# Performance work log

Hardware: AMD Instinct MI355X
Metric: run time of the kernel (lower is better)

The kernel has to match this reference:

```python
import jax, jax.numpy as jnp
import numpy as np


def setup_inputs() -> dict:
    key = jax.random.key(0)
    kq, kk, kv = jax.random.split(key, 3)
    B, S, H, D = 2, 2048, 32, 128
    q = jax.random.normal(kq, (B, S, H, D), dtype=jnp.float32)
    k = jax.random.normal(kk, (B, S, H, D), dtype=jnp.float32)
    v = jax.random.normal(kv, (B, S, H, D), dtype=jnp.float32)
    return {"q": q, "k": k, "v": v}


def _causal_attention(q, k, v):
    # q,k,v: [B, S, H, D] (flash-attn layout). Zigzag ring attention computes
    # exactly standard causal attention; zigzag only balances work across ranks.
    B, S, H, D = q.shape
    scale = 1.0 / jnp.sqrt(jnp.asarray(D, q.dtype))
    scores = jnp.einsum('bqhd,bkhd->bhqk', q, k) * scale  # [B,H,S,S]
    causal = jnp.tril(jnp.ones((S, S), dtype=bool))
    scores = jnp.where(causal, scores, jnp.finfo(scores.dtype).min)
    probs = jax.nn.softmax(scores, axis=-1)
    return jnp.einsum('bhqk,bkhd->bqhd', probs, v)  # [B,S,H,D]


def reference(q, k, v):
    out = _causal_attention(q, k, v)
    return jnp.sum(out)
```

## Files before the change

kernel.cpp:

```cpp
#include <hip/hip_runtime.h>
#include <hip/hip_bf16.h>
#include <stdint.h>

#define B_ 2
#define S_ 2048
#define H_ 32
#define D_ 128
#define R_ (B_*H_*S_)
#define QKB (B_ * S_ * (H_/8))
#define VSB (B_ * S_)
#define NDB (2 * R_ / 1024)
#define CPB 40

typedef __bf16 bf16x8 __attribute__((ext_vector_type(8)));
typedef float  f32x16 __attribute__((ext_vector_type(16)));

#if __has_builtin(__builtin_amdgcn_exp2f)
#define EXP2F(x) __builtin_amdgcn_exp2f(x)
#else
#define EXP2F(x) exp2f(x)
#endif

#define AS1 __attribute__((address_space(1)))
#define AS3 __attribute__((address_space(3)))

__device__ __forceinline__ unsigned short f2bf(float f) {
  unsigned u = __float_as_uint(f);
  u += 0x7FFFu + ((u >> 16) & 1u);
  return (unsigned short)(u >> 16);
}

__global__ __launch_bounds__(256) void prep(
    const float* __restrict__ q, const float* __restrict__ k,
    const float* __restrict__ v,
    unsigned short* __restrict__ qb, unsigned short* __restrict__ kb,
    float* __restrict__ vsum, float* __restrict__ nd, float* __restrict__ out0) {
  const int bid = blockIdx.x;
  const int t = threadIdx.x;
  if (bid == 0 && t == 0) out0[0] = 0.f;
  if (bid < 2 * QKB) {
    const int which = bid >= QKB;
    const int i2 = which ? bid - QKB : bid;
    const float* src = which ? k : q;
    unsigned short* dst = which ? kb : qb;
    const float sc = which ? 1.0f : 0.0883883476483184f * 1.4426950408889634f;
    const int b   = i2 / (S_ * 4);
    const int rem = i2 % (S_ * 4);
    const int s   = rem >> 2;
    const int h   = (rem & 3) * 8 + (t >> 5);
    const int lane32 = t & 31;
    const float4 v4 = *reinterpret_cast<const float4*>(
        src + (((size_t)b * S_ + s) * H_ + h) * D_ + lane32 * 4);
    ushort4 o;
    o.x = f2bf(v4.x * sc); o.y = f2bf(v4.y * sc);
    o.z = f2bf(v4.z * sc); o.w = f2bf(v4.w * sc);
    *reinterpret_cast<ushort4*>(
        dst + (((size_t)b * H_ + h) * S_ + s) * D_ + lane32 * 4) = o;
  } else if (bid < 2 * QKB + VSB) {
    const int i2 = bid - 2 * QKB;
    const int b = i2 / S_, s = i2 % S_;
    const int h = t >> 3, i = t & 7;
    const float* p = v + (((size_t)b * S_ + s) * H_ + h) * D_ + i * 16;
    const float4 a0 = *reinterpret_cast<const float4*>(p + 0);
    const float4 a1 = *reinterpret_cast<const float4*>(p + 4);
    const float4 a2 = *reinterpret_cast<const float4*>(p + 8);
    const float4 a3 = *reinterpret_cast<const float4*>(p + 12);
    float sum = (a0.x+a0.y+a0.z+a0.w) + (a1.x+a1.y+a1.z+a1.w)
              + (a2.x+a2.y+a2.z+a2.w) + (a3.x+a3.y+a3.z+a3.w);
    sum += __shfl_xor(sum, 1);
    sum += __shfl_xor(sum, 2);
    sum += __shfl_xor(sum, 4);
    if (i == 0) vsum[((size_t)b * H_ + h) * S_ + s] = sum;
  } else {
    float4* p = reinterpret_cast<float4*>(nd);
    p[(size_t)(bid - 2 * QKB - VSB) * 256 + t] = float4{0.f, 0.f, 0.f, 0.f};
  }
}

__global__ __launch_bounds__(256, 4) void attn_sum(
    const unsigned short* __restrict__ qg_, const unsigned short* __restrict__ kg_,
    const float* __restrict__ vsum, float* __restrict__ numb,
    float* __restrict__ denb) {
  __shared__ uint4 kbuf[2][1024];
  __shared__ float vsbuf[2][64];

  const int id = blockIdx.x;
  const int y  = id >> 3;
  const int bh = (id & 7) + 8 * (y / CPB);
  const int c  = y % CPB;

  int qt, h, nch;
  if (c < 4)       { qt = c;                 h = 0;            nch = 1; }
  else if (c < 12) { qt = 4 + ((c - 4) >> 1);  h = (c - 4) & 1;  nch = 2; }
  else if (c < 24) { qt = 8 + (c - 12) / 3;    h = (c - 12) % 3; nch = 3; }
  else             { qt = 12 + ((c - 24) >> 2); h = (c - 24) & 3; nch = 4; }
  const int nkt  = 2 * qt + 2;
  const int bas_ = nkt / nch, rem = nkt % nch;
  const int kt0  = h * bas_ + (h < rem ? h : rem);
  const int kt1  = kt0 + bas_ + (h < rem ? 1 : 0);

  const int t  = threadIdx.x;
  const int w  = t >> 6;
  const int l  = t & 63;
  const int ln = l & 31, l5 = l >> 5;

  const size_t base = (size_t)bh * S_ * D_;
  const int qrow0 = qt * 128 + w * 32;
  const unsigned short* ksrc0 = kg_ + base;
  const float* vsrc0 = vsum + (size_t)bh * S_;

  bf16x8 qfrag[8];
  {
    const unsigned short* qp = qg_ + base + (size_t)(qrow0 + ln) * D_ + l5 * 8;
    #pragma unroll
    for (int kb8 = 0; kb8 < 8; ++kb8)
      qfrag[kb8] = *reinterpret_cast<const bf16x8*>(qp + kb8 * 16);
  }

  auto stage = [&](int j, int slot) {
    const unsigned short* ksrc = ksrc0 + (size_t)j * 64 * D_;
    #pragma unroll
    for (int i = 0; i < 4; ++i) {
      const int idx = w * 256 + i * 64 + l;
      const int r   = idx >> 4;
      const int p   = idx & 15;
      const int cc  = p ^ (r & 15);
      const unsigned short* src = ksrc + r * D_ + cc * 8;
      __builtin_amdgcn_global_load_lds(
          (const AS1 void*)src, (AS3 void*)(&kbuf[slot][idx & ~63]), 16, 0, 0);
    }
    __builtin_amdgcn_global_load_lds(
        (const AS1 void*)(vsrc0 + j * 64 + l), (AS3 void*)(&vsbuf[slot][0]), 4, 0, 0);
  };

  float num[16], den[16];
  #pragma unroll
  for (int r = 0; r < 16; ++r) { num[r] = 0.f; den[r] = 0.f; }

  stage(kt0, 0);
  int cur = 0;
  const int xr = ln & 15;
  for (int kt = kt0; kt < kt1; ++kt) {
    asm volatile("s_waitcnt vmcnt(0)" ::: "memory");
    __syncthreads();
    if (kt + 1 < kt1) stage(kt + 1, cur ^ 1);

    const int ktb = kt * 64;
    if (ktb <= qrow0 + 31) {
      #pragma unroll
      for (int nb = 0; nb < 2; ++nb) {
        const int kbase = ktb + nb * 32;
        if (kbase > qrow0 + 31) continue;
        const uint4* rowb = &kbuf[cur][(nb * 32 + ln) * 16];
        f32x16 sacc = {0.f,0.f,0.f,0.f,0.f,0.f,0.f,0.f,
                       0.f,0.f,0.f,0.f,0.f,0.f,0.f,0.f};
        __builtin_amdgcn_s_setprio(1);
        #pragma unroll
        for (int kb8 = 0; kb8 < 8; ++kb8) {
          const bf16x8 bf = *reinterpret_cast<const bf16x8*>(&rowb[(kb8 * 2 + l5) ^ xr]);
          sacc = __builtin_amdgcn_mfma_f32_32x32x16_bf16(qfrag[kb8], bf, sacc, 0, 0, 0);
        }
        __builtin_amdgcn_s_setprio(0);
        const float vsv = vsbuf[cur][nb * 32 + ln];
        if (kbase + 31 <= qrow0) {
          #pragma unroll
          for (int r = 0; r < 16; ++r) {
            const float e = EXP2F(sacc[r]);
            den[r] += e;
            num[r] = fmaf(e, vsv, num[r]);
          }
        } else {
          const int kgc = kbase + ln;
          #pragma unroll
          for (int r = 0; r < 16; ++r) {
            const int qgr = qrow0 + (r & 3) + 8 * (r >> 2) + 4 * l5;
            const float e = (kgc <= qgr) ? EXP2F(sacc[r]) : 0.f;
            den[r] += e;
            num[r] = fmaf(e, vsv, num[r]);
          }
        }
      }
    }
    cur ^= 1;
  }

  #pragma unroll
  for (int m = 1; m < 32; m <<= 1) {
    #pragma unroll
    for (int r = 0; r < 16; ++r) {
      num[r] += __shfl_xor(num[r], m);
      den[r] += __shfl_xor(den[r], m);
    }
  }
  if (ln == 0) {
    float* nrow = numb + (size_t)bh * S_;
    float* drow = denb + (size_t)bh * S_;
    #pragma unroll
    for (int r = 0; r < 16; ++r) {
      const int qgr = qrow0 + (r & 3) + 8 * (r >> 2) + 4 * l5;
      atomicAdd(&nrow[qgr], num[r]);
      atomicAdd(&drow[qgr], den[r]);
    }
  }
}

__global__ __launch_bounds__(256) void finalize(
    const float* __restrict__ numb, const float* __restrict__ denb,
    float* __restrict__ out) {
  const int i = blockIdx.x * 256 + threadIdx.x;
  float c = numb[i] / denb[i];
  #pragma unroll
  for (int m = 1; m < 64; m <<= 1) c += __shfl_xor(c, m);
  __shared__ float ps[4];
  if ((threadIdx.x & 63) == 0) ps[threadIdx.x >> 6] = c;
  __syncthreads();
  if (threadIdx.x == 0) atomicAdd(out, ps[0] + ps[1] + ps[2] + ps[3]);
}

extern "C" void kernel_launch(void* const* d_in, const int* in_sizes, int n_in,
                              void* d_out, int out_size, void* d_ws, size_t ws_size,
                              hipStream_t stream) {
  const float* q = (const float*)d_in[0];
  const float* k = (const float*)d_in[1];
  const float* v = (const float*)d_in[2];
  float* out = (float*)d_out;

  unsigned short* qb = (unsigned short*)d_ws;
  unsigned short* kb = qb + (size_t)R_ * D_;
  float* vsum = (float*)(kb + (size_t)R_ * D_);
  float* numb = vsum + R_;
  float* denb = numb + R_;

  hipLaunchKernelGGL(prep, dim3(2 * QKB + VSB + NDB), dim3(256), 0, stream,
                     q, k, v, qb, kb, vsum, numb, out);
  hipLaunchKernelGGL(attn_sum, dim3(64 * CPB), dim3(256), 0, stream,
                     qb, kb, vsum, numb, denb);
  hipLaunchKernelGGL(finalize, dim3(R_ / 256), dim3(256), 0, stream,
                     numb, denb, out);
}
```

Baseline: 114.4 us.

## Use 4-slot 32-row K pipeline with partial waits and grid-stride prep kernel

```diff
diff --git a/kernel.cpp b/kernel.cpp
--- a/kernel.cpp
+++ b/kernel.cpp
@@ -7,9 +7,9 @@
 #define H_ 32
 #define D_ 128
 #define R_ (B_*H_*S_)
-#define QKB (B_ * S_ * (H_/8))
-#define VSB (B_ * S_)
-#define NDB (2 * R_ / 1024)
+#define PG 2048
+#define QKU (2 * B_ * S_ * (H_/8))
+#define VSU (B_ * S_)
 #define CPB 40
 
 typedef __bf16 bf16x8 __attribute__((ext_vector_type(8)));
@@ -38,9 +38,12 @@
   const int bid = blockIdx.x;
   const int t = threadIdx.x;
   if (bid == 0 && t == 0) out0[0] = 0.f;
-  if (bid < 2 * QKB) {
-    const int which = bid >= QKB;
-    const int i2 = which ? bid - QKB : bid;
+
+  #pragma unroll 4
+  for (int g = 0; g < QKU / PG; ++g) {
+    const int u = bid + g * PG;
+    const int which = u >= (QKU / 2);
+    const int i2 = which ? u - (QKU / 2) : u;
     const float* src = which ? k : q;
     unsigned short* dst = which ? kb : qb;
     const float sc = which ? 1.0f : 0.0883883476483184f * 1.4426950408889634f;
@@ -56,9 +59,12 @@
     o.z = f2bf(v4.z * sc); o.w = f2bf(v4.w * sc);
     *reinterpret_cast<ushort4*>(
         dst + (((size_t)b * H_ + h) * S_ + s) * D_ + lane32 * 4) = o;
-  } else if (bid < 2 * QKB + VSB) {
-    const int i2 = bid - 2 * QKB;
-    const int b = i2 / S_, s = i2 % S_;
+  }
+
+  #pragma unroll
+  for (int g = 0; g < VSU / PG; ++g) {
+    const int u = bid + g * PG;
+    const int b = u / S_, s = u % S_;
     const int h = t >> 3, i = t & 7;
     const float* p = v + (((size_t)b * S_ + s) * H_ + h) * D_ + i * 16;
     const float4 a0 = *reinterpret_cast<const float4*>(p + 0);
@@ -71,9 +77,11 @@
     sum += __shfl_xor(sum, 2);
     sum += __shfl_xor(sum, 4);
     if (i == 0) vsum[((size_t)b * H_ + h) * S_ + s] = sum;
-  } else {
+  }
+
+  if (bid < 256) {
     float4* p = reinterpret_cast<float4*>(nd);
-    p[(size_t)(bid - 2 * QKB - VSB) * 256 + t] = float4{0.f, 0.f, 0.f, 0.f};
+    p[(size_t)bid * 256 + t] = float4{0.f, 0.f, 0.f, 0.f};
   }
 }
 
@@ -81,8 +89,8 @@
     const unsigned short* __restrict__ qg_, const unsigned short* __restrict__ kg_,
     const float* __restrict__ vsum, float* __restrict__ numb,
     float* __restrict__ denb) {
-  __shared__ uint4 kbuf[2][1024];
-  __shared__ float vsbuf[2][64];
+  __shared__ uint4 kbuf[4][512];
+  __shared__ float vsbuf[4][64];
 
   const int id = blockIdx.x;
   const int y  = id >> 3;
@@ -98,6 +106,7 @@
   const int bas_ = nkt / nch, rem = nkt % nch;
   const int kt0  = h * bas_ + (h < rem ? h : rem);
   const int kt1  = kt0 + bas_ + (h < rem ? 1 : 0);
+  const int st0  = 2 * kt0, st1 = 2 * kt1;
 
   const int t  = threadIdx.x;
   const int w  = t >> 6;
@@ -117,11 +126,11 @@
       qfrag[kb8] = *reinterpret_cast<const bf16x8*>(qp + kb8 * 16);
   }
 
-  auto stage = [&](int j, int slot) {
-    const unsigned short* ksrc = ksrc0 + (size_t)j * 64 * D_;
-    #pragma unroll
-    for (int i = 0; i < 4; ++i) {
-      const int idx = w * 256 + i * 64 + l;
+  auto stage = [&](int st, int slot) {
+    const unsigned short* ksrc = ksrc0 + (size_t)st * 32 * D_;
+    #pragma unroll
+    for (int j = 0; j < 2; ++j) {
+      const int idx = (w * 2 + j) * 64 + l;
       const int r   = idx >> 4;
       const int p   = idx & 15;
       const int cc  = p ^ (r & 15);
@@ -130,58 +139,55 @@
           (const AS1 void*)src, (AS3 void*)(&kbuf[slot][idx & ~63]), 16, 0, 0);
     }
     __builtin_amdgcn_global_load_lds(
-        (const AS1 void*)(vsrc0 + j * 64 + l), (AS3 void*)(&vsbuf[slot][0]), 4, 0, 0);
+        (const AS1 void*)(vsrc0 + st * 32 + l), (AS3 void*)(&vsbuf[slot][0]), 4, 0, 0);
   };
 
   float num[16], den[16];
   #pragma unroll
   for (int r = 0; r < 16; ++r) { num[r] = 0.f; den[r] = 0.f; }
 
-  stage(kt0, 0);
-  int cur = 0;
+  stage(st0, st0 & 3);
+  stage(st0 + 1, (st0 + 1) & 3);
+
   const int xr = ln & 15;
-  for (int kt = kt0; kt < kt1; ++kt) {
-    asm volatile("s_waitcnt vmcnt(0)" ::: "memory");
-    __syncthreads();
-    if (kt + 1 < kt1) stage(kt + 1, cur ^ 1);
-
-    const int ktb = kt * 64;
-    if (ktb <= qrow0 + 31) {
+  for (int st = st0; st < st1; ++st) {
+    if (st + 1 < st1) asm volatile("s_waitcnt vmcnt(3)" ::: "memory");
+    else              asm volatile("s_waitcnt vmcnt(0)" ::: "memory");
+    __builtin_amdgcn_s_barrier();
+    if (st + 2 < st1) stage(st + 2, (st + 2) & 3);
+
+    const int kbase = st * 32;
+    if (kbase <= qrow0 + 31) {
+      const int slot = st & 3;
+      const uint4* rowb = &kbuf[slot][ln * 16];
+      f32x16 sacc = {0.f,0.f,0.f,0.f,0.f,0.f,0.f,0.f,
+                     0.f,0.f,0.f,0.f,0.f,0.f,0.f,0.f};
+      __builtin_amdgcn_s_setprio(1);
       #pragma unroll
-      for (int nb = 0; nb < 2; ++nb) {
-        const int kbase = ktb + nb * 32;
-        if (kbase > qrow0 + 31) continue;
-        const uint4* rowb = &kbuf[cur][(nb * 32 + ln) * 16];
-        f32x16 sacc = {0.f,0.f,0.f,0.f,0.f,0.f,0.f,0.f,
-                       0.f,0.f,0.f,0.f,0.f,0.f,0.f,0.f};
-        __builtin_amdgcn_s_setprio(1);
+      for (int kb8 = 0; kb8 < 8; ++kb8) {
+        const bf16x8 bf = *reinterpret_cast<const bf16x8*>(&rowb[(kb8 * 2 + l5) ^ xr]);
+        sacc = __builtin_amdgcn_mfma_f32_32x32x16_bf16(qfrag[kb8], bf, sacc, 0, 0, 0);
+      }
+      __builtin_amdgcn_s_setprio(0);
+      const float vsv = vsbuf[slot][ln];
+      if (kbase + 31 <= qrow0) {
         #pragma unroll
-        for (int kb8 = 0; kb8 < 8; ++kb8) {
-          const bf16x8 bf = *reinterpret_cast<const bf16x8*>(&rowb[(kb8 * 2 + l5) ^ xr]);
-          sacc = __builtin_amdgcn_mfma_f32_32x32x16_bf16(qfrag[kb8], bf, sacc, 0, 0, 0);
+        for (int r = 0; r < 16; ++r) {
+          const float e = EXP2F(sacc[r]);
+          den[r] += e;
+          num[r] = fmaf(e, vsv, num[r]);
         }
-        __builtin_amdgcn_s_setprio(0);
-        const float vsv = vsbuf[cur][nb * 32 + ln];
-        if (kbase + 31 <= qrow0) {
-          #pragma unroll
-          for (int r = 0; r < 16; ++r) {
-            const float e = EXP2F(sacc[r]);
-            den[r] += e;
-            num[r] = fmaf(e, vsv, num[r]);
-          }
-        } else {
-          const int kgc = kbase + ln;
-          #pragma unroll
-          for (int r = 0; r < 16; ++r) {
-            const int qgr = qrow0 + (r & 3) + 8 * (r >> 2) + 4 * l5;
-            const float e = (kgc <= qgr) ? EXP2F(sacc[r]) : 0.f;
-            den[r] += e;
-            num[r] = fmaf(e, vsv, num[r]);
-          }
+      } else {
+        const int kgc = kbase + ln;
+        #pragma unroll
+        for (int r = 0; r < 16; ++r) {
+          const int qgr = qrow0 + (r & 3) + 8 * (r >> 2) + 4 * l5;
+          const float e = (kgc <= qgr) ? EXP2F(sacc[r]) : 0.f;
+          den[r] += e;
+          num[r] = fmaf(e, vsv, num[r]);
         }
       }
     }
-    cur ^= 1;
   }
 
   #pragma unroll
@@ -231,7 +237,7 @@
   float* numb = vsum + R_;
   float* denb = numb + R_;
 
-  hipLaunchKernelGGL(prep, dim3(2 * QKB + VSB + NDB), dim3(256), 0, stream,
+  hipLaunchKernelGGL(prep, dim3(PG), dim3(256), 0, stream,
                      q, k, v, qb, kb, vsum, numb, out);
   hipLaunchKernelGGL(attn_sum, dim3(64 * CPB), dim3(256), 0, stream,
                      qb, kb, vsum, numb, denb);
```

After: 120.5 us. 5.3% more time.
